# Optimization experiments

Hardware: AMD Instinct MI355X
Metric: run time of the kernel (lower is better)

## Reference

```python
import jax, jax.numpy as jnp
import numpy as np
import math

B, T, H, W, C = 2, 8, 32, 32, 512
DEPTH = 2
HEADS = 16
GH = 8            # global FAVOR+ heads (first GH heads, as in performer-pytorch)
DH = C // HEADS   # 32
WIN = C // 8      # 64 = local window size
FF = 2 * C
NB_F = int(DH * math.log(DH))  # 110 random features (performer default)


def _ortho_proj(m, d, rng):
    # gaussian orthogonal random matrix, scaling=0 (row norms ~ chi(d))
    blocks = []
    for _ in range(m // d + 1):
        q, _ = np.linalg.qr(rng.standard_normal((d, d)))
        blocks.append(q.T)
    Q = np.concatenate(blocks, 0)[:m]
    mult = np.linalg.norm(rng.standard_normal((m, d)), axis=1)
    return (mult[:, None] * Q).astype(np.float32)


def setup_inputs():
    rng = np.random.default_rng(0)
    g = lambda *s: jnp.asarray(rng.standard_normal(s) * 0.02, jnp.float32)
    z = lambda *s: jnp.zeros(s, jnp.float32)
    o = lambda *s: jnp.ones(s, jnp.float32)
    p = {}
    p["x"] = jnp.asarray(rng.standard_normal((B, T, H, W, C)), jnp.float32)
    p["ln1_g"], p["ln1_b"] = o(DEPTH, C), z(DEPTH, C)
    p["Wq"], p["bq"] = g(DEPTH, C, C), z(DEPTH, C)
    p["Wk"], p["bk"] = g(DEPTH, C, C), z(DEPTH, C)
    p["Wv"], p["bv"] = g(DEPTH, C, C), z(DEPTH, C)
    p["Wo"], p["bo"] = g(DEPTH, C, C), z(DEPTH, C)
    p["proj"] = jnp.asarray(np.stack([_ortho_proj(NB_F, DH, rng) for _ in range(DEPTH)]))
    p["ln2_g"], p["ln2_b"] = o(DEPTH, C), z(DEPTH, C)
    p["W1"], p["b1"] = g(DEPTH, C, FF), z(DEPTH, FF)
    p["W2"], p["b2"] = g(DEPTH, FF, C), z(DEPTH, C)
    return p


def _ln(x, g, b):
    m = x.mean(-1, keepdims=True)
    v = x.var(-1, keepdims=True)
    return (x - m) / jnp.sqrt(v + 1e-5) * g + b


def _softmax_kernel(x, proj, is_query):
    # FAVOR+ positive softmax features. x: [b,h,n,d], proj: [m,d]
    d = x.shape[-1]
    m = proj.shape[0]
    dn = d ** -0.25
    dd = jnp.einsum('bhnd,md->bhnm', x * dn, proj)
    diag = jnp.sum(x * x, -1, keepdims=True) * 0.5 * (dn * dn)
    if is_query:
        stab = jnp.max(dd, axis=-1, keepdims=True)
    else:
        stab = jnp.max(dd, axis=(-1, -2), keepdims=True)
    return (m ** -0.5) * (jnp.exp(dd - diag - stab) + 1e-4)


def _rot_half(x):
    x1, x2 = jnp.split(x, 2, axis=-1)
    return jnp.concatenate([-x2, x1], axis=-1)


def _local_attn(q, k, v, win=WIN):
    # non-causal sliding window, look_backward=1, look_forward=1
    b, hh, n, d = q.shape
    nw = n // win
    qb = q.reshape(b, hh, nw, win, d)
    kb = k.reshape(b, hh, nw, win, d)
    vb = v.reshape(b, hh, nw, win, d)

    def look(t):
        p = jnp.pad(t, ((0, 0), (0, 0), (1, 1), (0, 0), (0, 0)))
        return jnp.concatenate([p[:, :, :-2], p[:, :, 1:-1], p[:, :, 2:]], 3)

    kk, vv = look(kb), look(vb)
    posb = jnp.arange(n).reshape(nw, win)
    pp = jnp.pad(posb, ((1, 1), (0, 0)), constant_values=-1)
    kpos = jnp.concatenate([pp[:-2], pp[1:-1], pp[2:]], 1)
    mask = (kpos == -1)[None, None, :, None, :]
    s = jnp.einsum('bhwid,bhwjd->bhwij', qb * (d ** -0.5), kk)
    s = jnp.where(mask, -1e9, s)
    a = jax.nn.softmax(s, axis=-1)
    o = jnp.einsum('bhwij,bhwjd->bhwid', a, vv)
    return o.reshape(b, hh, n, d)


def _forward(x, ln1_g, ln1_b, Wq, bq, Wk, bk, Wv, bv, Wo, bo, proj, ln2_g, ln2_b, W1, b1, W2, b2):
    Bx, Tx, Hx, Wx, Cx = x.shape
    n = Tx * Hx * Wx
    h = x.reshape(Bx, n, Cx)
    # rotary rel-pos for local heads (local-attention rel_pos_emb_config)
    inv_freq = 1.0 / (10000.0 ** (jnp.arange(0, DH, 2, dtype=jnp.float32) / DH))
    freqs = jnp.arange(n, dtype=jnp.float32)[:, None] * inv_freq[None, :]
    emb = jnp.concatenate([freqs, freqs], -1)
    sin, cos = jnp.sin(emb), jnp.cos(emb)

    for l in range(DEPTH):
        y = _ln(h, ln1_g[l], ln1_b[l])
        q = (y @ Wq[l] + bq[l]).reshape(Bx, n, HEADS, DH).transpose(0, 2, 1, 3)
        k = (y @ Wk[l] + bk[l]).reshape(Bx, n, HEADS, DH).transpose(0, 2, 1, 3)
        v = (y @ Wv[l] + bv[l]).reshape(Bx, n, HEADS, DH).transpose(0, 2, 1, 3)
        gq, lq = q[:, :GH], q[:, GH:]
        gk, lk = k[:, :GH], k[:, GH:]
        gv, lv = v[:, :GH], v[:, GH:]
        # global: FAVOR+ linear attention
        qp = _softmax_kernel(gq, proj[l], True)
        kp = _softmax_kernel(gk, proj[l], False)
        Dinv = 1.0 / jnp.einsum('bhnm,bhm->bhn', qp, kp.sum(-2))
        ctx = jnp.einsum('bhnm,bhnd->bhmd', kp, gv)
        og = jnp.einsum('bhmd,bhnm,bhn->bhnd', ctx, qp, Dinv)
        # local: windowed attention with rotary pos emb
        lqr = lq * cos + _rot_half(lq) * sin
        lkr = lk * cos + _rot_half(lk) * sin
        ol = _local_attn(lqr, lkr, lv)
        o = jnp.concatenate([og, ol], 1).transpose(0, 2, 1, 3).reshape(Bx, n, Cx)
        h = h + o @ Wo[l] + bo[l]
        y = _ln(h, ln2_g[l], ln2_b[l])
        h = h + jax.nn.gelu(y @ W1[l] + b1[l], approximate=False) @ W2[l] + b2[l]
    return h.reshape(Bx, Tx, Hx, Wx, Cx)


def reference(x, ln1_g, ln1_b, Wq, bq, Wk, bk, Wv, bv, Wo, bo, proj, ln2_g, ln2_b, W1, b1, W2, b2):
    return _forward(x, ln1_g, ln1_b, Wq, bq, Wk, bk, Wv, bv, Wo, bo, proj, ln2_g, ln2_b, W1, b1, W2, b2)
```

## Files before the change

kernel.cpp:

```cpp
#include <hip/hip_runtime.h>
#include <math.h>

namespace {

constexpr int BATCH = 2;
constexpr int NTOK  = 8192;
constexpr int MROWS = 16384;
constexpr int C     = 512;
constexpr int GH    = 8;
constexpr int DH    = 32;
constexpr int WIN   = 64;
constexpr int NW    = 128;
constexpr int FF    = 1024;
constexpr int NBF   = 110;
constexpr int NBFP  = 128;

constexpr float F_DN     = 0.42044820762685725f;
constexpr float F_RNORM  = 0.09534625892455924f;
constexpr float F_LSCALE = 0.17677669529663687f;

typedef __attribute__((ext_vector_type(8))) short bf16x8;
typedef __attribute__((ext_vector_type(4))) float f32x4;

__device__ __forceinline__ ushort f2b(float f){
  unsigned u = __float_as_uint(f);
  unsigned r = u + 0x7FFFu + ((u >> 16) & 1u);
  return (ushort)(r >> 16);
}
__device__ __forceinline__ float b2f(ushort u){
  return __uint_as_float((unsigned)u << 16);
}

__device__ __forceinline__ void gload16(const void* g, void* l){
  __builtin_amdgcn_global_load_lds((const __attribute__((address_space(1))) void*)g,
                                   (__attribute__((address_space(3))) void*)l, 16, 0, 0);
}

__global__ void k_tables(float* __restrict__ cost, float* __restrict__ sint){
  int idx = blockIdx.x*256 + threadIdx.x;
  if (idx >= NTOK*16) return;
  int pos = idx >> 4, f = idx & 15;
  float inv = powf(10000.f, -(float)f/16.f);
  float ang = (float)pos * inv;
  cost[idx] = cosf(ang);
  sint[idx] = sinf(ang);
}

__global__ __launch_bounds__(256) void k_wcvt_all(const float* __restrict__ Wq, const float* __restrict__ Wk,
     const float* __restrict__ Wv, const float* __restrict__ Wo, const float* __restrict__ W1,
     const float* __restrict__ W2, ushort* __restrict__ wt){
  __shared__ float t[32][33];
  int id = blockIdx.x;
  int l = id >> 11;
  int r = id & 2047;
  const float* src; ushort* dst; int K, N, bx, by;
  if (r < 1024){
    int mat = r >> 8, tt = r & 255;
    bx = tt & 15; by = tt >> 4; K = 512; N = 512;
    src = ((mat == 0) ? Wq : (mat == 1) ? Wk : (mat == 2) ? Wv : Wo) + (size_t)l*262144;
    dst = wt + (size_t)l*2097152 + (size_t)mat*262144;
  } else if (r < 1536){
    int tt = r - 1024;
    bx = tt & 31; by = tt >> 5; K = 512; N = 1024;
    src = W1 + (size_t)l*524288;
    dst = wt + (size_t)l*2097152 + 1048576;
  } else {
    int tt = r - 1536;
    bx = tt & 15; by = tt >> 4; K = 1024; N = 512;
    src = W2 + (size_t)l*524288;
    dst = wt + (size_t)l*2097152 + 1572864;
  }
  int tx = threadIdx.x & 31, ty = threadIdx.x >> 5;
  #pragma unroll
  for (int rr = ty; rr < 32; rr += 8) t[rr][tx] = src[(size_t)(by*32+rr)*N + bx*32 + tx];
  __syncthreads();
  #pragma unroll
  for (int rr = ty; rr < 32; rr += 8) dst[(size_t)(bx*32+rr)*K + by*32 + tx] = f2b(t[tx][rr]);
}

template<int INBF>
__global__ __launch_bounds__(256) void k_ln(const void* __restrict__ xv, const float* __restrict__ g,
                     const float* __restrict__ b, ushort* __restrict__ y){
  int row = blockIdx.x, t = threadIdx.x;
  float2 v;
  if (INBF){
    ushort2 u = *(const ushort2*)((const ushort*)xv + (size_t)row*C + 2*t);
    v.x = b2f(u.x); v.y = b2f(u.y);
  } else {
    v = *(const float2*)((const float*)xv + (size_t)row*C + 2*t);
  }
  float s = v.x + v.y, ss = v.x*v.x + v.y*v.y;
  #pragma unroll
  for (int o = 32; o; o >>= 1){ s += __shfl_down(s, o); ss += __shfl_down(ss, o); }
  __shared__ float rs[4], rss[4];
  int wv = t >> 6, ln = t & 63;
  if (ln == 0){ rs[wv] = s; rss[wv] = ss; }
  __syncthreads();
  float S = rs[0]+rs[1]+rs[2]+rs[3], SS = rss[0]+rss[1]+rss[2]+rss[3];
  float mean = S * (1.f/C);
  float var  = SS * (1.f/C) - mean*mean;
  float rstd = rsqrtf(var + 1e-5f);
  float2 gg = *(const float2*)(g + 2*t);
  float2 bb = *(const float2*)(b + 2*t);
  ushort2 ov;
  ov.x = f2b((v.x - mean)*rstd*gg.x + bb.x);
  ov.y = f2b((v.y - mean)*rstd*gg.y + bb.y);
  *(ushort2*)(y + (size_t)row*C + 2*t) = ov;
}

template<int ACT, int OBF, int QKV, int RESBF>
__global__ __launch_bounds__(512) void k_mgemm(const ushort* __restrict__ A, const ushort* __restrict__ Bt,
      const float* __restrict__ bias, const float* __restrict__ bias2, const float* __restrict__ bias3,
      const void* __restrict__ res, float* __restrict__ outf, ushort* __restrict__ outb,
      const float* __restrict__ cosT, const float* __restrict__ sinT, int Nd, int Kd){
  __shared__ ushort As[2][256*32];
  __shared__ ushort Bs[2][128*32];
  int tid = threadIdx.x;
  int lane = tid & 63, wave = tid >> 6;
  int c = lane & 15, g = lane >> 4;
  int wr = wave >> 1, wc = wave & 1;
  int gx = gridDim.x;
  int nwg = gx * (int)gridDim.y;
  int bid = (int)(blockIdx.y*gx + blockIdx.x);
  int swz = (bid & 7)*(nwg >> 3) + (bid >> 3);
  int row0 = (swz / gx)*256, col0 = (swz % gx)*128;
  f32x4 acc[4][4] = {};
  int nt = Kd >> 5;

  #define STAGE(buf, kt) {                                                        \
    int k0_ = (kt)*32;                                                            \
    _Pragma("unroll")                                                             \
    for (int j = 0; j < 2; j++){                                                  \
      int ci = j*512 + tid;                                                       \
      gload16(A + (size_t)(row0 + (ci>>2))*Kd + k0_ + (ci&3)*8,                   \
              (char*)As[buf] + (j*512 + wave*64)*16);                             \
    }                                                                             \
    {                                                                             \
      int ci = tid;                                                               \
      gload16(Bt + (size_t)(col0 + (ci>>2))*Kd + k0_ + (ci&3)*8,                  \
              (char*)Bs[buf] + (wave*64)*16);                                     \
    }                                                                             \
  }

  STAGE(0, 0);
  __syncthreads();

  for (int t = 0; t < nt; t++){
    int cur = t & 1;
    bf16x8 af[4], bfr[4];
    #pragma unroll
    for (int m = 0; m < 4; m++)
      af[m] = *(const bf16x8*)(As[cur] + (wr*64 + m*16 + c)*32 + g*8);
    #pragma unroll
    for (int n = 0; n < 4; n++)
      bfr[n] = *(const bf16x8*)(Bs[cur] + (wc*64 + n*16 + c)*32 + g*8);
    if (t + 1 < nt) STAGE(cur^1, t+1);
    __builtin_amdgcn_s_setprio(1);
    #pragma unroll
    for (int m = 0; m < 4; m++)
      #pragma unroll
      for (int n = 0; n < 4; n++)
        acc[m][n] = __builtin_amdgcn_mfma_f32_16x16x32_bf16(af[m], bfr[n], acc[m][n], 0, 0, 0);
    __builtin_amdgcn_s_setprio(0);
    __syncthreads();
  }
  #undef STAGE

  if (QKV){
    #pragma unroll
    for (int m = 0; m < 4; m++){
      int rbase = row0 + wr*64 + m*16 + g*4;
      #pragma unroll
      for (int np = 0; np < 2; np++){
        int n0 = 2*np, n1 = n0 + 1;
        int ccol = col0 + wc*64 + n0*16 + c;
        int bid2 = ccol >> 9;
        int cl  = ccol & 511;
        const float* bp = (bid2 == 0) ? bias : (bid2 == 1) ? bias2 : bias3;
        float b0 = bp[cl], b1 = bp[cl+16];
        bool dorope = (bid2 < 2) && (cl >= 256);
        ushort* obase = outb + (size_t)bid2*MROWS*C;
        #pragma unroll
        for (int r = 0; r < 4; r++){
          int grow = rbase + r;
          float a  = acc[m][n0][r] + b0;
          float bb = acc[m][n1][r] + b1;
          if (dorope){
            int pos = grow & (NTOK-1);
            float cv = cosT[pos*16 + c], sv = sinT[pos*16 + c];
            float na = a*cv - bb*sv;
            float nb = bb*cv + a*sv;
            a = na; bb = nb;
          }
          obase[(size_t)grow*C + cl]      = f2b(a);
          obase[(size_t)grow*C + cl + 16] = f2b(bb);
        }
      }
    }
    return;
  }
  #pragma unroll
  for (int m = 0; m < 4; m++){
    int rbase = row0 + wr*64 + m*16 + g*4;
    #pragma unroll
    for (int n = 0; n < 4; n++){
      int ccol = col0 + wc*64 + n*16 + c;
      float bv = bias[ccol];
      #pragma unroll
      for (int r = 0; r < 4; r++){
        int grow = rbase + r;
        float vv = acc[m][n][r] + bv;
        if (ACT == 1) vv = 0.5f*vv*(1.f + erff(vv*0.7071067811865476f));
        if (res){
          size_t ri = (size_t)grow*Nd + ccol;
          vv += RESBF ? b2f(((const ushort*)res)[ri]) : ((const float*)res)[ri];
        }
        if (OBF) outb[(size_t)grow*Nd + ccol] = f2b(vv);
        else     outf[(size_t)grow*Nd + ccol] = vv;
      }
    }
  }
}

template<int ACT, int OBF, int RESBF>
__global__ __launch_bounds__(256) void k_mgemm_s(const ushort* __restrict__ A, const ushort* __restrict__ Bt,
      const float* __restrict__ bias, const void* __restrict__ res,
      float* __restrict__ outf, ushort* __restrict__ outb, int Nd, int Kd){
  __shared__ ushort As[2][128*32];
  __shared__ ushort Bs[2][128*32];
  int tid = threadIdx.x;
  int lane = tid & 63, wave = tid >> 6;
  int wr = wave >> 1, wc = wave & 1;
  int gx = gridDim.x;
  int nwg = gx * (int)gridDim.y;
  int bid = (int)(blockIdx.y*gx + blockIdx.x);
  int swz = (bid & 7)*(nwg >> 3) + (bid >> 3);
  int row0 = (swz / gx)*128, col0 = (swz % gx)*128;
  f32x4 acc[4][4] = {};
  int nt = Kd >> 5;

  #define STAGE(buf, kt) {                                                        \
    int k0_ = (kt)*32;                                                            \
    _Pragma("unroll")                                                             \
    for (int cc = 0; cc < 2; cc++){                                               \
      int off = (wave*2 + cc)*1024 + lane*16;                                     \
      int r_ = off >> 6, ke_ = (off & 63) >> 1;                                   \
      gload16(A  + (size_t)(row0 + r_)*Kd + k0_ + ke_,                            \
              (char*)As[buf] + (wave*2 + cc)*1024);                               \
      gload16(Bt + (size_t)(col0 + r_)*Kd + k0_ + ke_,                            \
              (char*)Bs[buf] + (wave*2 + cc)*1024);                               \
    }                                                                             \
  }

  STAGE(0, 0);
  __syncthreads();

  for (int t = 0; t < nt; t++){
    int cur = t & 1;
    bf16x8 af[4], bfr[4];
    #pragma unroll
    for (int m = 0; m < 4; m++)
      af[m] = *(const bf16x8*)((const char*)As[cur] + (wr*64 + m*16 + (lane&15))*64 + (lane>>4)*16);
    #pragma unroll
    for (int n = 0; n < 4; n++)
      bfr[n] = *(const bf16x8*)((const char*)Bs[cur] + (wc*64 + n*16 + (lane&15))*64 + (lane>>4)*16);
    if (t + 1 < nt) STAGE(cur^1, t+1);
    __builtin_amdgcn_s_setprio(1);
    #pragma unroll
    for (int m = 0; m < 4; m++)
      #pragma unroll
      for (int n = 0; n < 4; n++)
        acc[m][n] = __builtin_amdgcn_mfma_f32_16x16x32_bf16(af[m], bfr[n], acc[m][n], 0, 0, 0);
    __builtin_amdgcn_s_setprio(0);
    __syncthreads();
  }
  #undef STAGE

  #pragma unroll
  for (int m = 0; m < 4; m++){
    int rbase = row0 + wr*64 + m*16 + (lane>>4)*4;
    #pragma unroll
    for (int n = 0; n < 4; n++){
      int ccol = col0 + wc*64 + n*16 + (lane&15);
      float bv = bias[ccol];
      #pragma unroll
      for (int r = 0; r < 4; r++){
        int grow = rbase + r;
        float vv = acc[m][n][r] + bv;
        if (ACT == 1) vv = 0.5f*vv*(1.f + erff(vv*0.7071067811865476f));
        if (res){
          size_t ri = (size_t)grow*Nd + ccol;
          vv += RESBF ? b2f(((const ushort*)res)[ri]) : ((const float*)res)[ri];
        }
        if (OBF) outb[(size_t)grow*Nd + ccol] = f2b(vv);
        else     outf[(size_t)grow*Nd + ccol] = vv;
      }
    }
  }
}

__global__ __launch_bounds__(256) void k_ctx3(const ushort* __restrict__ k, const ushort* __restrict__ v,
        const float* __restrict__ proj, float* __restrict__ ctxp, float* __restrict__ ksump){
  int bh = blockIdx.x >> 5, chunk = blockIdx.x & 31;
  int b = bh >> 3, h = bh & 7;
  __shared__ __align__(16) ushort pl[NBFP*40];
  __shared__ __align__(16) ushort Ps[NBFP*72];
  __shared__ __align__(16) ushort Vt[48*72];
  __shared__ float dgl[256];
  int tid = threadIdx.x;
  int lane = tid & 63, wave = tid >> 6;
  int c = lane & 15, g = lane >> 4;
  int i0 = chunk*256;

  for (int idx = tid; idx < NBFP*32; idx += 256){
    int f = idx >> 5, d = idx & 31;
    pl[f*40 + d] = (f < NBF) ? f2b(proj[f*32 + d]*F_DN) : (ushort)0;
  }
  const ushort* kbase = k + ((size_t)b*NTOK + i0)*C + h*DH;
  const ushort* vbase = v + ((size_t)b*NTOK + i0)*C + h*DH;
  #pragma unroll
  for (int s = 0; s < 4; s++){
    bf16x8 kf = *(const bf16x8*)(kbase + (size_t)(s*64 + wave*16 + c)*C + g*8);
    const ushort* kp_ = (const ushort*)&kf;
    float sq = 0.f;
    #pragma unroll
    for (int j = 0; j < 8; j++){ float vv = b2f(kp_[j]); sq += vv*vv; }
    sq += __shfl_xor(sq, 16);
    sq += __shfl_xor(sq, 32);
    if (g == 0) dgl[s*64 + wave*16 + c] = 0.5f*F_DN*F_DN*sq;
  }
  for (int idx = tid; idx < 15*72; idx += 256) Vt[33*72 + idx] = 0;

  f32x4 zz = {0.f, 0.f, 0.f, 0.f};
  f32x4 acc[2][3] = {};

  for (int s = 0; s < 4; s++){
    __syncthreads();
    {
      int r = tid >> 2, part = tid & 3;
      uint4 vv = *(const uint4*)(vbase + (size_t)(s*64 + r)*C + part*8);
      const ushort* vp = (const ushort*)&vv;
      #pragma unroll
      for (int j = 0; j < 8; j++) Vt[(part*8+j)*72 + r] = vp[j];
      if (tid < 64) Vt[32*72 + tid] = 0x3F80;
    }
    bf16x8 af = *(const bf16x8*)(kbase + (size_t)(s*64 + wave*16 + c)*C + g*8);
    #pragma unroll
    for (int ft = 0; ft < 8; ft++){
      bf16x8 bf = *(const bf16x8*)(pl + (ft*16 + c)*40 + g*8);
      f32x4 dd = __builtin_amdgcn_mfma_f32_16x16x32_bf16(af, bf, zz, 0, 0, 0);
      int feat = ft*16 + c;
      bool fvalid = feat < NBF;
      ushort pb[4];
      #pragma unroll
      for (int r = 0; r < 4; r++){
        float kp = 0.f;
        if (fvalid){
          float dg_ = dgl[s*64 + wave*16 + g*4 + r];
          kp = F_RNORM*(__expf(dd[r] - dg_) + 1e-4f);
        }
        pb[r] = f2b(kp);
      }
      uint2 pd;
      pd.x = (unsigned)pb[0] | ((unsigned)pb[1] << 16);
      pd.y = (unsigned)pb[2] | ((unsigned)pb[3] << 16);
      *(uint2*)(Ps + (ft*16 + c)*72 + wave*16 + g*4) = pd;
    }
    __syncthreads();
    #pragma unroll
    for (int i = 0; i < 2; i++){
      int ft = wave*2 + i;
      #pragma unroll
      for (int kk = 0; kk < 2; kk++){
        bf16x8 ap = *(const bf16x8*)(Ps + (ft*16 + c)*72 + kk*32 + g*8);
        #pragma unroll
        for (int nt = 0; nt < 3; nt++){
          bf16x8 bv = *(const bf16x8*)(Vt + (nt*16 + c)*72 + kk*32 + g*8);
          acc[i][nt] = __builtin_amdgcn_mfma_f32_16x16x32_bf16(ap, bv, acc[i][nt], 0, 0, 0);
        }
      }
    }
  }
  size_t pbase = (size_t)(bh*32 + chunk)*NBF;
  #pragma unroll
  for (int i = 0; i < 2; i++){
    int ftb = (wave*2 + i)*16;
    #pragma unroll
    for (int r = 0; r < 4; r++){
      int feat = ftb + g*4 + r;
      if (feat < NBF){
        #pragma unroll
        for (int nt = 0; nt < 2; nt++)
          ctxp[(pbase + feat)*DH + nt*16 + c] = acc[i][nt][r];
        if (c == 0) ksump[pbase + feat] = acc[i][2][r];
      }
    }
  }
}

__global__ void k_ctxred(const float* __restrict__ ctxp, const float* __restrict__ ksump,
                         float* __restrict__ ctx, float* __restrict__ ksum){
  int bh = blockIdx.x / NBF, m = blockIdx.x % NBF;
  int t = threadIdx.x;
  if (t < DH){
    float s = 0.f;
    for (int c = 0; c < 32; c++) s += ctxp[((size_t)(bh*32 + c)*NBF + m)*DH + t];
    ctx[((size_t)bh*NBF + m)*DH + t] = s;
  } else if (t == DH){
    float s = 0.f;
    for (int c = 0; c < 32; c++) s += ksump[(size_t)(bh*32 + c)*NBF + m];
    ksum[bh*NBF + m] = s;
  }
}

__global__ __launch_bounds__(256) void k_qattn3(const ushort* __restrict__ q, const float* __restrict__ proj,
        const float* __restrict__ ctx, const float* __restrict__ ksum, ushort* __restrict__ o){
  int bh = blockIdx.x >> 7, chunk = blockIdx.x & 127;
  int b = bh >> 3, h = bh & 7;
  __shared__ __align__(16) ushort pl[NBFP*40];
  __shared__ __align__(16) ushort ql[64*40];
  __shared__ __align__(16) ushort ctl[32*136];
  __shared__ __align__(16) ushort Ps[64*136];
  __shared__ float ksl[NBFP];
  __shared__ float dgl[64];
  __shared__ float dvl[64];
  int tid = threadIdx.x;
  int lane = tid & 63, wave = tid >> 6;
  int c = lane & 15, g = lane >> 4;
  int i0 = chunk*64;

  for (int idx = tid; idx < NBFP*32; idx += 256){
    int f = idx >> 5, d = idx & 31;
    pl[f*40 + d] = (f < NBF) ? f2b(proj[f*32 + d]*F_DN) : (ushort)0;
  }
  {
    int row = tid >> 2, part = tid & 3;
    uint4 qq = *(const uint4*)(q + (size_t)(b*NTOK + i0 + row)*C + h*DH + part*8);
    *(uint4*)(ql + row*40 + part*8) = qq;
    const ushort* qp_ = (const ushort*)&qq;
    float sq = 0.f;
    #pragma unroll
    for (int j = 0; j < 8; j++){ float vv = b2f(qp_[j]); sq += vv*vv; }
    sq += __shfl_xor(sq, 1);
    sq += __shfl_xor(sq, 2);
    if (part == 0) dgl[row] = 0.5f*F_DN*F_DN*sq;
  }
  for (int idx = tid; idx < 32*NBFP; idx += 256){
    int d = idx >> 7, f = idx & 127;
    float vv = (f < NBF) ? ctx[((size_t)bh*NBF + f)*DH + d] : 0.f;
    ctl[d*136 + f] = f2b(vv);
  }
  if (tid < NBFP) ksl[tid] = (tid < NBF) ? ksum[bh*NBF + tid] : 0.f;
  __syncthreads();

  f32x4 zz = {0.f, 0.f, 0.f, 0.f};
  bf16x8 qf = *(const bf16x8*)(ql + (wave*16 + c)*40 + g*8);
  f32x4 st[8];
  #pragma unroll
  for (int mt = 0; mt < 8; mt++){
    bf16x8 af = *(const bf16x8*)(pl + (mt*16 + c)*40 + g*8);
    st[mt] = __builtin_amdgcn_mfma_f32_16x16x32_bf16(af, qf, zz, 0, 0, 0);
  }
  float mx = -1e30f;
  #pragma unroll
  for (int mt = 0; mt < 8; mt++)
    #pragma unroll
    for (int r = 0; r < 4; r++){
      int feat = mt*16 + g*4 + r;
      if (feat < NBF) mx = fmaxf(mx, st[mt][r]);
    }
  mx = fmaxf(mx, __shfl_xor(mx, 16));
  mx = fmaxf(mx, __shfl_xor(mx, 32));
  float diagv = dgl[wave*16 + c];
  float dv = 0.f;
  #pragma unroll
  for (int mt = 0; mt < 8; mt++){
    ushort pb[4];
    #pragma unroll
    for (int r = 0; r < 4; r++){
      int feat = mt*16 + g*4 + r;
      float qp = 0.f;
      if (feat < NBF) qp = F_RNORM*(__expf(st[mt][r] - diagv - mx) + 1e-4f);
      ushort qb = f2b(qp);
      pb[r] = qb;
      dv += b2f(qb)*ksl[feat];
    }
    uint2 pd;
    pd.x = (unsigned)pb[0] | ((unsigned)pb[1] << 16);
    pd.y = (unsigned)pb[2] | ((unsigned)pb[3] << 16);
    *(uint2*)(Ps + (wave*16 + c)*136 + mt*16 + g*4) = pd;
  }
  dv += __shfl_xor(dv, 16);
  dv += __shfl_xor(dv, 32);
  if (g == 0) dvl[wave*16 + c] = 1.f/dv;
  __syncthreads();

  #pragma unroll
  for (int n = 0; n < 2; n++){
    f32x4 acc = zz;
    #pragma unroll
    for (int kk = 0; kk < 4; kk++){
      bf16x8 ap = *(const bf16x8*)(Ps  + (wave*16 + c)*136 + kk*32 + g*8);
      bf16x8 bc = *(const bf16x8*)(ctl + (n*16 + c)*136    + kk*32 + g*8);
      acc = __builtin_amdgcn_mfma_f32_16x16x32_bf16(ap, bc, acc, 0, 0, 0);
    }
    #pragma unroll
    for (int r = 0; r < 4; r++){
      int qrow = wave*16 + g*4 + r;
      float val = acc[r]*dvl[qrow];
      o[(size_t)(b*NTOK + i0 + qrow)*C + h*DH + n*16 + c] = f2b(val);
    }
  }
}

__global__ __launch_bounds__(256) void k_local2(const ushort* __restrict__ q, const ushort* __restrict__ k,
        const ushort* __restrict__ v, ushort* __restrict__ o){
  int blk = blockIdx.x;
  int w = blk & (NW-1);
  int rem = blk >> 7;
  int hl = rem & 7, b = rem >> 3;
  int hd = GH + hl;
  __shared__ __align__(16) ushort Ks[192*32];
  __shared__ __align__(16) ushort Vt[32*200];
  __shared__ __align__(16) ushort Ps[4*16*200];
  int tid = threadIdx.x;
  int lane = tid & 63, wave = tid >> 6;
  int c = lane & 15, g = lane >> 4;

  const ushort* kbase = k + (size_t)b*NTOK*C + hd*DH;
  const ushort* vbase = v + (size_t)b*NTOK*C + hd*DH;
  #pragma unroll
  for (int s = 0; s < 3; s++){
    int ch = tid + s*256;
    int row = ch >> 2, part = ch & 3;
    int kp = min(max((w-1)*WIN + row, 0), NTOK-1);
    gload16(kbase + (size_t)kp*C + part*8, (char*)Ks + (s*256 + wave*64)*16);
  }
  #pragma unroll
  for (int s = 0; s < 3; s++){
    int ch = tid + s*256;
    int row = ch >> 2, part = ch & 3;
    int kp = min(max((w-1)*WIN + row, 0), NTOK-1);
    uint4 vv = *(const uint4*)(vbase + (size_t)kp*C + part*8);
    const ushort* vp = (const ushort*)&vv;
    #pragma unroll
    for (int j = 0; j < 8; j++) Vt[(part*8+j)*200 + row] = vp[j];
  }
  int qrow = w*WIN + wave*16 + c;
  bf16x8 qf = *(const bf16x8*)(q + ((size_t)b*NTOK + qrow)*C + hd*DH + g*8);
  asm volatile("s_waitcnt vmcnt(0)" ::: "memory");
  __syncthreads();

  f32x4 zz = {0.f, 0.f, 0.f, 0.f};
  f32x4 st[12];
  #pragma unroll
  for (int t = 0; t < 12; t++){
    bf16x8 af = *(const bf16x8*)(Ks + (16*t + c)*32 + g*8);
    st[t] = __builtin_amdgcn_mfma_f32_16x16x32_bf16(af, qf, zz, 0, 0, 0);
  }
  int t0 = (w == 0) ? 4 : 0;
  int t1 = (w == NW-1) ? 8 : 12;
  float lsum = 0.f;
  ushort* pw = Ps + wave*3200 + c*200;
  #pragma unroll
  for (int t = 0; t < 12; t++){
    bool valid = (t >= t0) && (t < t1);
    float p0 = valid ? __expf(st[t][0]*F_LSCALE) : 0.f;
    float p1 = valid ? __expf(st[t][1]*F_LSCALE) : 0.f;
    float p2 = valid ? __expf(st[t][2]*F_LSCALE) : 0.f;
    float p3 = valid ? __expf(st[t][3]*F_LSCALE) : 0.f;
    lsum += (p0+p1)+(p2+p3);
    uint2 pd;
    pd.x = (unsigned)f2b(p0) | ((unsigned)f2b(p1) << 16);
    pd.y = (unsigned)f2b(p2) | ((unsigned)f2b(p3) << 16);
    *(uint2*)(pw + 16*t + 4*g) = pd;
  }
  lsum += __shfl_xor(lsum, 16);
  lsum += __shfl_xor(lsum, 32);

  f32x4 oc0 = zz, oc1 = zz;
  #pragma unroll
  for (int kb = 0; kb < 6; kb++){
    bf16x8 pf = *(const bf16x8*)(pw + kb*32 + g*8);
    bf16x8 v0 = *(const bf16x8*)(Vt + c*200 + kb*32 + g*8);
    bf16x8 v1 = *(const bf16x8*)(Vt + (16 + c)*200 + kb*32 + g*8);
    oc0 = __builtin_amdgcn_mfma_f32_16x16x32_bf16(v0, pf, oc0, 0, 0, 0);
    oc1 = __builtin_amdgcn_mfma_f32_16x16x32_bf16(v1, pf, oc1, 0, 0, 0);
  }
  float inv = 1.f/lsum;
  ushort* orow = o + ((size_t)b*NTOK + qrow)*C + hd*DH;
  uint2 w0, w1;
  w0.x = (unsigned)f2b(oc0[0]*inv) | ((unsigned)f2b(oc0[1]*inv) << 16);
  w0.y = (unsigned)f2b(oc0[2]*inv) | ((unsigned)f2b(oc0[3]*inv) << 16);
  w1.x = (unsigned)f2b(oc1[0]*inv) | ((unsigned)f2b(oc1[1]*inv) << 16);
  w1.y = (unsigned)f2b(oc1[2]*inv) | ((unsigned)f2b(oc1[3]*inv) << 16);
  *(uint2*)(orow + 4*g)      = w0;
  *(uint2*)(orow + 16 + 4*g) = w1;
}

}

extern "C" void kernel_launch(void* const* d_in, const int* in_sizes, int n_in,
                              void* d_out, int out_size, void* d_ws, size_t ws_size,
                              hipStream_t stream){
  (void)in_sizes; (void)n_in; (void)out_size; (void)ws_size;
  const float* x     = (const float*)d_in[0];
  const float* ln1_g = (const float*)d_in[1];
  const float* ln1_b = (const float*)d_in[2];
  const float* Wq    = (const float*)d_in[3];
  const float* bq    = (const float*)d_in[4];
  const float* Wk    = (const float*)d_in[5];
  const float* bk    = (const float*)d_in[6];
  const float* Wv    = (const float*)d_in[7];
  const float* bv    = (const float*)d_in[8];
  const float* Wo    = (const float*)d_in[9];
  const float* bo    = (const float*)d_in[10];
  const float* proj  = (const float*)d_in[11];
  const float* ln2_g = (const float*)d_in[12];
  const float* ln2_b = (const float*)d_in[13];
  const float* W1    = (const float*)d_in[14];
  const float* b1    = (const float*)d_in[15];
  const float* W2    = (const float*)d_in[16];
  const float* b2    = (const float*)d_in[17];

  float* h = (float*)d_out;
  const size_t MC = (size_t)MROWS*C;
  char* w = (char*)d_ws;
  auto alloc = [&](size_t bytes)->char*{ char* p = w; w += (bytes + 255) & ~(size_t)255; return p; };

  ushort* y16  = (ushort*)alloc(MC*2);
  ushort* qb16 = (ushort*)alloc(MC*2);
  ushort* kb16 = (ushort*)alloc(MC*2);
  ushort* vb16 = (ushort*)alloc(MC*2);
  ushort* o16  = (ushort*)alloc(MC*2);
  ushort* h16  = (ushort*)alloc(MC*2);
  ushort* wt   = (ushort*)alloc((size_t)2*2097152*2);
  float*  cost = (float*) alloc((size_t)NTOK*16*4);
  float*  sint = (float*) alloc((size_t)NTOK*16*4);
  float*  ctxb = (float*) alloc((size_t)16*NBF*DH*4);
  float*  ksum = (float*) alloc((size_t)16*NBF*4);

  ushort* mid16 = qb16;
  float*  ctxp  = (float*)o16;
  float*  ksump = ctxp + (size_t)16*32*NBF*DH;

  k_tables<<<(NTOK*16 + 255)/256, 256, 0, stream>>>(cost, sint);
  k_wcvt_all<<<4096, 256, 0, stream>>>(Wq, Wk, Wv, Wo, W1, W2, wt);

  dim3 blkg(512);
  dim3 blks(256);
  dim3 g512s(4, 128);
  dim3 gqkv(12, 64);
  dim3 gff(8, 64);

  for (int l = 0; l < 2; l++){
    const float* pj = proj + (size_t)l*NBF*DH;
    ushort* wl  = wt + (size_t)l*2097152;
    ushort* wtq = wl;
    ushort* wto = wl +  786432;
    ushort* wt1 = wl + 1048576;
    ushort* wt2 = wl + 1572864;

    if (l == 0) k_ln<0><<<MROWS, 256, 0, stream>>>(x,   ln1_g + l*C, ln1_b + l*C, y16);
    else        k_ln<1><<<MROWS, 256, 0, stream>>>(h16, ln1_g + l*C, ln1_b + l*C, y16);
    k_mgemm<0,1,1,0><<<gqkv, blkg, 0, stream>>>(y16, wtq, bq + l*C, bk + l*C, bv + l*C,
                                                nullptr, nullptr, qb16, cost, sint, 1536, C);
    k_ctx3<<<16*32, 256, 0, stream>>>(kb16, vb16, pj, ctxp, ksump);
    k_ctxred<<<16*NBF, 64, 0, stream>>>(ctxp, ksump, ctxb, ksum);
    k_qattn3<<<16*128, 256, 0, stream>>>(qb16, pj, ctxb, ksum, o16);
    k_local2<<<BATCH*8*NW, 256, 0, stream>>>(qb16, kb16, vb16, o16);
    if (l == 0)
      k_mgemm_s<0,1,0><<<g512s, blks, 0, stream>>>(o16, wto, bo + l*C, x, nullptr, h16, C, C);
    else
      k_mgemm_s<0,1,1><<<g512s, blks, 0, stream>>>(o16, wto, bo + l*C, h16, nullptr, h16, C, C);
    k_ln<1><<<MROWS, 256, 0, stream>>>(h16, ln2_g + l*C, ln2_b + l*C, y16);
    k_mgemm<1,1,0,0><<<gff, blkg, 0, stream>>>(y16, wt1, b1 + l*FF, nullptr, nullptr, nullptr,
                                               nullptr, mid16, nullptr, nullptr, FF, C);
    if (l == 0)
      k_mgemm_s<0,1,1><<<g512s, blks, 0, stream>>>(mid16, wt2, b2 + l*C, h16, nullptr, h16, C, FF);
    else
      k_mgemm_s<0,0,1><<<g512s, blks, 0, stream>>>(mid16, wt2, b2 + l*C, h16, h, nullptr, C, FF);
  }
}
```

Baseline: 477.4 us.

## Merge FAVOR+ context kernel and local window attention into one launch

The global-head context-partial kernel and the local windowed attention kernel are combined into a single launch. Block index selects the branch, and the two branches share one shared-memory buffer. The ctx partials move out of the o16 buffer into their own workspace allocation, since the local branch now writes o16 concurrently. The aim is to remove one launch and let the small ctx grid overlap with the local attention blocks, at the cost of the larger combined shared-memory footprint applying to every block.

```diff
diff --git a/kernel.cpp b/kernel.cpp
--- a/kernel.cpp
+++ b/kernel.cpp
@@ -299,102 +299,187 @@
   }
 }
 
-__global__ __launch_bounds__(256) void k_ctx3(const ushort* __restrict__ k, const ushort* __restrict__ v,
-        const float* __restrict__ proj, float* __restrict__ ctxp, float* __restrict__ ksump){
-  int bh = blockIdx.x >> 5, chunk = blockIdx.x & 31;
-  int b = bh >> 3, h = bh & 7;
-  __shared__ __align__(16) ushort pl[NBFP*40];
-  __shared__ __align__(16) ushort Ps[NBFP*72];
-  __shared__ __align__(16) ushort Vt[48*72];
-  __shared__ float dgl[256];
+__global__ __launch_bounds__(256) void k_attn_pair(const ushort* __restrict__ q,
+        const ushort* __restrict__ k, const ushort* __restrict__ v,
+        const float* __restrict__ proj, float* __restrict__ ctxp, float* __restrict__ ksump,
+        ushort* __restrict__ o){
+  __shared__ __align__(16) char smem[50688];
   int tid = threadIdx.x;
   int lane = tid & 63, wave = tid >> 6;
   int c = lane & 15, g = lane >> 4;
-  int i0 = chunk*256;
-
-  for (int idx = tid; idx < NBFP*32; idx += 256){
-    int f = idx >> 5, d = idx & 31;
-    pl[f*40 + d] = (f < NBF) ? f2b(proj[f*32 + d]*F_DN) : (ushort)0;
-  }
-  const ushort* kbase = k + ((size_t)b*NTOK + i0)*C + h*DH;
-  const ushort* vbase = v + ((size_t)b*NTOK + i0)*C + h*DH;
-  #pragma unroll
-  for (int s = 0; s < 4; s++){
-    bf16x8 kf = *(const bf16x8*)(kbase + (size_t)(s*64 + wave*16 + c)*C + g*8);
-    const ushort* kp_ = (const ushort*)&kf;
-    float sq = 0.f;
-    #pragma unroll
-    for (int j = 0; j < 8; j++){ float vv = b2f(kp_[j]); sq += vv*vv; }
-    sq += __shfl_xor(sq, 16);
-    sq += __shfl_xor(sq, 32);
-    if (g == 0) dgl[s*64 + wave*16 + c] = 0.5f*F_DN*F_DN*sq;
-  }
-  for (int idx = tid; idx < 15*72; idx += 256) Vt[33*72 + idx] = 0;
-
-  f32x4 zz = {0.f, 0.f, 0.f, 0.f};
-  f32x4 acc[2][3] = {};
-
-  for (int s = 0; s < 4; s++){
-    __syncthreads();
-    {
-      int r = tid >> 2, part = tid & 3;
-      uint4 vv = *(const uint4*)(vbase + (size_t)(s*64 + r)*C + part*8);
-      const ushort* vp = (const ushort*)&vv;
-      #pragma unroll
-      for (int j = 0; j < 8; j++) Vt[(part*8+j)*72 + r] = vp[j];
-      if (tid < 64) Vt[32*72 + tid] = 0x3F80;
-    }
-    bf16x8 af = *(const bf16x8*)(kbase + (size_t)(s*64 + wave*16 + c)*C + g*8);
-    #pragma unroll
-    for (int ft = 0; ft < 8; ft++){
-      bf16x8 bf = *(const bf16x8*)(pl + (ft*16 + c)*40 + g*8);
-      f32x4 dd = __builtin_amdgcn_mfma_f32_16x16x32_bf16(af, bf, zz, 0, 0, 0);
-      int feat = ft*16 + c;
-      bool fvalid = feat < NBF;
-      ushort pb[4];
-      #pragma unroll
-      for (int r = 0; r < 4; r++){
-        float kp = 0.f;
-        if (fvalid){
-          float dg_ = dgl[s*64 + wave*16 + g*4 + r];
-          kp = F_RNORM*(__expf(dd[r] - dg_) + 1e-4f);
+
+  if (blockIdx.x < 512){
+    ushort* pl  = (ushort*)smem;
+    ushort* Ps  = (ushort*)(smem + 10240);
+    ushort* Vt  = (ushort*)(smem + 28672);
+    float*  dgl = (float*) (smem + 35584);
+    int bh = blockIdx.x >> 5, chunk = blockIdx.x & 31;
+    int b = bh >> 3, h = bh & 7;
+    int i0 = chunk*256;
+
+    for (int idx = tid; idx < NBFP*32; idx += 256){
+      int f = idx >> 5, d = idx & 31;
+      pl[f*40 + d] = (f < NBF) ? f2b(proj[f*32 + d]*F_DN) : (ushort)0;
+    }
+    const ushort* kbase = k + ((size_t)b*NTOK + i0)*C + h*DH;
+    const ushort* vbase = v + ((size_t)b*NTOK + i0)*C + h*DH;
+    #pragma unroll
+    for (int s = 0; s < 4; s++){
+      bf16x8 kf = *(const bf16x8*)(kbase + (size_t)(s*64 + wave*16 + c)*C + g*8);
+      const ushort* kp_ = (const ushort*)&kf;
+      float sq = 0.f;
+      #pragma unroll
+      for (int j = 0; j < 8; j++){ float vv = b2f(kp_[j]); sq += vv*vv; }
+      sq += __shfl_xor(sq, 16);
+      sq += __shfl_xor(sq, 32);
+      if (g == 0) dgl[s*64 + wave*16 + c] = 0.5f*F_DN*F_DN*sq;
+    }
+    for (int idx = tid; idx < 15*72; idx += 256) Vt[33*72 + idx] = 0;
+
+    f32x4 zz = {0.f, 0.f, 0.f, 0.f};
+    f32x4 acc[2][3] = {};
+
+    for (int s = 0; s < 4; s++){
+      __syncthreads();
+      {
+        int r = tid >> 2, part = tid & 3;
+        uint4 vv = *(const uint4*)(vbase + (size_t)(s*64 + r)*C + part*8);
+        const ushort* vp = (const ushort*)&vv;
+        #pragma unroll
+        for (int j = 0; j < 8; j++) Vt[(part*8+j)*72 + r] = vp[j];
+        if (tid < 64) Vt[32*72 + tid] = 0x3F80;
+      }
+      bf16x8 af = *(const bf16x8*)(kbase + (size_t)(s*64 + wave*16 + c)*C + g*8);
+      #pragma unroll
+      for (int ft = 0; ft < 8; ft++){
+        bf16x8 bf = *(const bf16x8*)(pl + (ft*16 + c)*40 + g*8);
+        f32x4 dd = __builtin_amdgcn_mfma_f32_16x16x32_bf16(af, bf, zz, 0, 0, 0);
+        int feat = ft*16 + c;
+        bool fvalid = feat < NBF;
+        ushort pb[4];
+        #pragma unroll
+        for (int r = 0; r < 4; r++){
+          float kp = 0.f;
+          if (fvalid){
+            float dg_ = dgl[s*64 + wave*16 + g*4 + r];
+            kp = F_RNORM*(__expf(dd[r] - dg_) + 1e-4f);
+          }
+          pb[r] = f2b(kp);
         }
-        pb[r] = f2b(kp);
+        uint2 pd;
+        pd.x = (unsigned)pb[0] | ((unsigned)pb[1] << 16);
+        pd.y = (unsigned)pb[2] | ((unsigned)pb[3] << 16);
+        *(uint2*)(Ps + (ft*16 + c)*72 + wave*16 + g*4) = pd;
       }
-      uint2 pd;
-      pd.x = (unsigned)pb[0] | ((unsigned)pb[1] << 16);
-      pd.y = (unsigned)pb[2] | ((unsigned)pb[3] << 16);
-      *(uint2*)(Ps + (ft*16 + c)*72 + wave*16 + g*4) = pd;
-    }
-    __syncthreads();
-    #pragma unroll
-    for (int i = 0; i < 2; i++){
-      int ft = wave*2 + i;
-      #pragma unroll
-      for (int kk = 0; kk < 2; kk++){
-        bf16x8 ap = *(const bf16x8*)(Ps + (ft*16 + c)*72 + kk*32 + g*8);
+      __syncthreads();
+      #pragma unroll
+      for (int i = 0; i < 2; i++){
+        int ft = wave*2 + i;
         #pragma unroll
-        for (int nt = 0; nt < 3; nt++){
-          bf16x8 bv = *(const bf16x8*)(Vt + (nt*16 + c)*72 + kk*32 + g*8);
-          acc[i][nt] = __builtin_amdgcn_mfma_f32_16x16x32_bf16(ap, bv, acc[i][nt], 0, 0, 0);
+        for (int kk = 0; kk < 2; kk++){
+          bf16x8 ap = *(const bf16x8*)(Ps + (ft*16 + c)*72 + kk*32 + g*8);
+          #pragma unroll
+          for (int nt = 0; nt < 3; nt++){
+            bf16x8 bv = *(const bf16x8*)(Vt + (nt*16 + c)*72 + kk*32 + g*8);
+            acc[i][nt] = __builtin_amdgcn_mfma_f32_16x16x32_bf16(ap, bv, acc[i][nt], 0, 0, 0);
+          }
         }
       }
     }
-  }
-  size_t pbase = (size_t)(bh*32 + chunk)*NBF;
-  #pragma unroll
-  for (int i = 0; i < 2; i++){
-    int ftb = (wave*2 + i)*16;
-    #pragma unroll
-    for (int r = 0; r < 4; r++){
-      int feat = ftb + g*4 + r;
-      if (feat < NBF){
-        #pragma unroll
-        for (int nt = 0; nt < 2; nt++)
-          ctxp[(pbase + feat)*DH + nt*16 + c] = acc[i][nt][r];
-        if (c == 0) ksump[pbase + feat] = acc[i][2][r];
+    size_t pbase = (size_t)(bh*32 + chunk)*NBF;
+    #pragma unroll
+    for (int i = 0; i < 2; i++){
+      int ftb = (wave*2 + i)*16;
+      #pragma unroll
+      for (int r = 0; r < 4; r++){
+        int feat = ftb + g*4 + r;
+        if (feat < NBF){
+          #pragma unroll
+          for (int nt = 0; nt < 2; nt++)
+            ctxp[(pbase + feat)*DH + nt*16 + c] = acc[i][nt][r];
+          if (c == 0) ksump[pbase + feat] = acc[i][2][r];
+        }
       }
     }
+  } else {
+    ushort* Ks = (ushort*)smem;
+    ushort* Vt = (ushort*)(smem + 12288);
+    ushort* Ps = (ushort*)(smem + 25088);
+    int blk = (int)blockIdx.x - 512;
+    int w = blk & (NW-1);
+    int rem = blk >> 7;
+    int hl = rem & 7, b = rem >> 3;
+    int hd = GH + hl;
+
+    const ushort* kbase = k + (size_t)b*NTOK*C + hd*DH;
+    const ushort* vbase = v + (size_t)b*NTOK*C + hd*DH;
+    #pragma unroll
+    for (int s = 0; s < 3; s++){
+      int ch = tid + s*256;
+      int row = ch >> 2, part = ch & 3;
+      int kp = min(max((w-1)*WIN + row, 0), NTOK-1);
+      gload16(kbase + (size_t)kp*C + part*8, (char*)Ks + (s*256 + wave*64)*16);
+    }
+    #pragma unroll
+    for (int s = 0; s < 3; s++){
+      int ch = tid + s*256;
+      int row = ch >> 2, part = ch & 3;
+      int kp = min(max((w-1)*WIN + row, 0), NTOK-1);
+      uint4 vv = *(const uint4*)(vbase + (size_t)kp*C + part*8);
+      const ushort* vp = (const ushort*)&vv;
+      #pragma unroll
+      for (int j = 0; j < 8; j++) Vt[(part*8+j)*200 + row] = vp[j];
+    }
+    int qrow = w*WIN + wave*16 + c;
+    bf16x8 qf = *(const bf16x8*)(q + ((size_t)b*NTOK + qrow)*C + hd*DH + g*8);
+    asm volatile("s_waitcnt vmcnt(0)" ::: "memory");
+    __syncthreads();
+
+    f32x4 zz = {0.f, 0.f, 0.f, 0.f};
+    f32x4 st[12];
+    #pragma unroll
+    for (int t = 0; t < 12; t++){
+      bf16x8 af = *(const bf16x8*)(Ks + (16*t + c)*32 + g*8);
+      st[t] = __builtin_amdgcn_mfma_f32_16x16x32_bf16(af, qf, zz, 0, 0, 0);
+    }
+    int t0 = (w == 0) ? 4 : 0;
+    int t1 = (w == NW-1) ? 8 : 12;
+    float lsum = 0.f;
+    ushort* pw = Ps + wave*3200 + c*200;
+    #pragma unroll
+    for (int t = 0; t < 12; t++){
+      bool valid = (t >= t0) && (t < t1);
+      float p0 = valid ? __expf(st[t][0]*F_LSCALE) : 0.f;
+      float p1 = valid ? __expf(st[t][1]*F_LSCALE) : 0.f;
+      float p2 = valid ? __expf(st[t][2]*F_LSCALE) : 0.f;
+      float p3 = valid ? __expf(st[t][3]*F_LSCALE) : 0.f;
+      lsum += (p0+p1)+(p2+p3);
+      uint2 pd;
+      pd.x = (unsigned)f2b(p0) | ((unsigned)f2b(p1) << 16);
+      pd.y = (unsigned)f2b(p2) | ((unsigned)f2b(p3) << 16);
+      *(uint2*)(pw + 16*t + 4*g) = pd;
+    }
+    lsum += __shfl_xor(lsum, 16);
+    lsum += __shfl_xor(lsum, 32);
+
+    f32x4 oc0 = zz, oc1 = zz;
+    #pragma unroll
+    for (int kb = 0; kb < 6; kb++){
+      bf16x8 pf = *(const bf16x8*)(pw + kb*32 + g*8);
+      bf16x8 v0 = *(const bf16x8*)(Vt + c*200 + kb*32 + g*8);
+      bf16x8 v1 = *(const bf16x8*)(Vt + (16 + c)*200 + kb*32 + g*8);
+      oc0 = __builtin_amdgcn_mfma_f32_16x16x32_bf16(v0, pf, oc0, 0, 0, 0);
+      oc1 = __builtin_amdgcn_mfma_f32_16x16x32_bf16(v1, pf, oc1, 0, 0, 0);
+    }
+    float inv = 1.f/lsum;
+    ushort* orow = o + ((size_t)b*NTOK + qrow)*C + hd*DH;
+    uint2 w0, w1;
+    w0.x = (unsigned)f2b(oc0[0]*inv) | ((unsigned)f2b(oc0[1]*inv) << 16);
+    w0.y = (unsigned)f2b(oc0[2]*inv) | ((unsigned)f2b(oc0[3]*inv) << 16);
+    w1.x = (unsigned)f2b(oc1[0]*inv) | ((unsigned)f2b(oc1[1]*inv) << 16);
+    w1.y = (unsigned)f2b(oc1[2]*inv) | ((unsigned)f2b(oc1[3]*inv) << 16);
+    *(uint2*)(orow + 4*g)      = w0;
+    *(uint2*)(orow + 16 + 4*g) = w1;
   }
 }
 
@@ -511,91 +596,6 @@
       o[(size_t)(b*NTOK + i0 + qrow)*C + h*DH + n*16 + c] = f2b(val);
     }
   }
-}
-
-__global__ __launch_bounds__(256) void k_local2(const ushort* __restrict__ q, const ushort* __restrict__ k,
-        const ushort* __restrict__ v, ushort* __restrict__ o){
-  int blk = blockIdx.x;
-  int w = blk & (NW-1);
-  int rem = blk >> 7;
-  int hl = rem & 7, b = rem >> 3;
-  int hd = GH + hl;
-  __shared__ __align__(16) ushort Ks[192*32];
-  __shared__ __align__(16) ushort Vt[32*200];
-  __shared__ __align__(16) ushort Ps[4*16*200];
-  int tid = threadIdx.x;
-  int lane = tid & 63, wave = tid >> 6;
-  int c = lane & 15, g = lane >> 4;
-
-  const ushort* kbase = k + (size_t)b*NTOK*C + hd*DH;
-  const ushort* vbase = v + (size_t)b*NTOK*C + hd*DH;
-  #pragma unroll
-  for (int s = 0; s < 3; s++){
-    int ch = tid + s*256;
-    int row = ch >> 2, part = ch & 3;
-    int kp = min(max((w-1)*WIN + row, 0), NTOK-1);
-    gload16(kbase + (size_t)kp*C + part*8, (char*)Ks + (s*256 + wave*64)*16);
-  }
-  #pragma unroll
-  for (int s = 0; s < 3; s++){
-    int ch = tid + s*256;
-    int row = ch >> 2, part = ch & 3;
-    int kp = min(max((w-1)*WIN + row, 0), NTOK-1);
-    uint4 vv = *(const uint4*)(vbase + (size_t)kp*C + part*8);
-    const ushort* vp = (const ushort*)&vv;
-    #pragma unroll
-    for (int j = 0; j < 8; j++) Vt[(part*8+j)*200 + row] = vp[j];
-  }
-  int qrow = w*WIN + wave*16 + c;
-  bf16x8 qf = *(const bf16x8*)(q + ((size_t)b*NTOK + qrow)*C + hd*DH + g*8);
-  asm volatile("s_waitcnt vmcnt(0)" ::: "memory");
-  __syncthreads();
-
-  f32x4 zz = {0.f, 0.f, 0.f, 0.f};
-  f32x4 st[12];
-  #pragma unroll
-  for (int t = 0; t < 12; t++){
-    bf16x8 af = *(const bf16x8*)(Ks + (16*t + c)*32 + g*8);
-    st[t] = __builtin_amdgcn_mfma_f32_16x16x32_bf16(af, qf, zz, 0, 0, 0);
-  }
-  int t0 = (w == 0) ? 4 : 0;
-  int t1 = (w == NW-1) ? 8 : 12;
-  float lsum = 0.f;
-  ushort* pw = Ps + wave*3200 + c*200;
-  #pragma unroll
-  for (int t = 0; t < 12; t++){
-    bool valid = (t >= t0) && (t < t1);
-    float p0 = valid ? __expf(st[t][0]*F_LSCALE) : 0.f;
-    float p1 = valid ? __expf(st[t][1]*F_LSCALE) : 0.f;
-    float p2 = valid ? __expf(st[t][2]*F_LSCALE) : 0.f;
-    float p3 = valid ? __expf(st[t][3]*F_LSCALE) : 0.f;
-    lsum += (p0+p1)+(p2+p3);
-    uint2 pd;
-    pd.x = (unsigned)f2b(p0) | ((unsigned)f2b(p1) << 16);
-    pd.y = (unsigned)f2b(p2) | ((unsigned)f2b(p3) << 16);
-    *(uint2*)(pw + 16*t + 4*g) = pd;
-  }
-  lsum += __shfl_xor(lsum, 16);
-  lsum += __shfl_xor(lsum, 32);
-
-  f32x4 oc0 = zz, oc1 = zz;
-  #pragma unroll
-  for (int kb = 0; kb < 6; kb++){
-    bf16x8 pf = *(const bf16x8*)(pw + kb*32 + g*8);
-    bf16x8 v0 = *(const bf16x8*)(Vt + c*200 + kb*32 + g*8);
-    bf16x8 v1 = *(const bf16x8*)(Vt + (16 + c)*200 + kb*32 + g*8);
-    oc0 = __builtin_amdgcn_mfma_f32_16x16x32_bf16(v0, pf, oc0, 0, 0, 0);
-    oc1 = __builtin_amdgcn_mfma_f32_16x16x32_bf16(v1, pf, oc1, 0, 0, 0);
-  }
-  float inv = 1.f/lsum;
-  ushort* orow = o + ((size_t)b*NTOK + qrow)*C + hd*DH;
-  uint2 w0, w1;
-  w0.x = (unsigned)f2b(oc0[0]*inv) | ((unsigned)f2b(oc0[1]*inv) << 16);
-  w0.y = (unsigned)f2b(oc0[2]*inv) | ((unsigned)f2b(oc0[3]*inv) << 16);
-  w1.x = (unsigned)f2b(oc1[0]*inv) | ((unsigned)f2b(oc1[1]*inv) << 16);
-  w1.y = (unsigned)f2b(oc1[2]*inv) | ((unsigned)f2b(oc1[3]*inv) << 16);
-  *(uint2*)(orow + 4*g)      = w0;
-  *(uint2*)(orow + 16 + 4*g) = w1;
 }
 
 }
@@ -639,10 +639,10 @@
   float*  sint = (float*) alloc((size_t)NTOK*16*4);
   float*  ctxb = (float*) alloc((size_t)16*NBF*DH*4);
   float*  ksum = (float*) alloc((size_t)16*NBF*4);
+  float*  ctxp = (float*) alloc((size_t)16*32*NBF*DH*4);
+  float*  ksump= (float*) alloc((size_t)16*32*NBF*4);
 
   ushort* mid16 = qb16;
-  float*  ctxp  = (float*)o16;
-  float*  ksump = ctxp + (size_t)16*32*NBF*DH;
 
   k_tables<<<(NTOK*16 + 255)/256, 256, 0, stream>>>(cost, sint);
   k_wcvt_all<<<4096, 256, 0, stream>>>(Wq, Wk, Wv, Wo, W1, W2, wt);
@@ -665,10 +665,9 @@
     else        k_ln<1><<<MROWS, 256, 0, stream>>>(h16, ln1_g + l*C, ln1_b + l*C, y16);
     k_mgemm<0,1,1,0><<<gqkv, blkg, 0, stream>>>(y16, wtq, bq + l*C, bk + l*C, bv + l*C,
                                                 nullptr, nullptr, qb16, cost, sint, 1536, C);
-    k_ctx3<<<16*32, 256, 0, stream>>>(kb16, vb16, pj, ctxp, ksump);
+    k_attn_pair<<<512 + BATCH*8*NW, 256, 0, stream>>>(qb16, kb16, vb16, pj, ctxp, ksump, o16);
     k_ctxred<<<16*NBF, 64, 0, stream>>>(ctxp, ksump, ctxb, ksum);
     k_qattn3<<<16*128, 256, 0, stream>>>(qb16, pj, ctxb, ksum, o16);
-    k_local2<<<BATCH*8*NW, 256, 0, stream>>>(qb16, kb16, vb16, o16);
     if (l == 0)
       k_mgemm_s<0,1,0><<<g512s, blks, 0, stream>>>(o16, wto, bo + l*C, x, nullptr, h16, C, C);
     else
```

Result: no change. 477.8 us (+0.1%).
